# Kernel optimization log

Hardware: AMD Instinct MI355X
Metric: run time of the kernel (lower is better)

Reference implementation:

```python
import jax, jax.numpy as jnp
import numpy as np

B, S, D = 2, 2048, 2048
H, HK, HD = 16, 4, 128          # query heads, kv heads, head dim (H*HD == D)
HID = 4 * D                      # SwiGLU hidden (mult=4)
WIN, SINK = 1024, 4              # sliding window, attention sink tokens
EPS = 1e-6
ROPE_BASE = 10000.0


def rmsnorm(x, g):
    return x * jax.lax.rsqrt(jnp.mean(x * x, axis=-1, keepdims=True) + EPS) * g


def rope_tables(seq_len, head_dim):
    inv = 1.0 / (ROPE_BASE ** (jnp.arange(0, head_dim, 2, dtype=jnp.float32) / head_dim))
    ang = jnp.arange(seq_len, dtype=jnp.float32)[:, None] * inv[None, :]  # [S, HD/2]
    return jnp.cos(ang), jnp.sin(ang)


def apply_rope(x, cos, sin):
    # x: [B, S, h, HD]; rotate-half convention
    x1, x2 = jnp.split(x, 2, axis=-1)
    c = cos[None, :, None, :]
    s = sin[None, :, None, :]
    return jnp.concatenate([x1 * c - x2 * s, x2 * c + x1 * s], axis=-1)


def setup_inputs() -> dict:
    key = jax.random.key(0)
    ks = jax.random.split(key, 10)
    p = 0.02
    return {
        "x": jax.random.normal(ks[0], (B, S, D), dtype=jnp.float32),
        "g1": jnp.ones((D,), dtype=jnp.float32),
        "g2": jnp.ones((D,), dtype=jnp.float32),
        "wq": jax.random.normal(ks[1], (D, H * HD), dtype=jnp.float32) * p,
        "wk": jax.random.normal(ks[2], (D, HK * HD), dtype=jnp.float32) * p,
        "wv": jax.random.normal(ks[3], (D, HK * HD), dtype=jnp.float32) * p,
        "wo": jax.random.normal(ks[4], (H * HD, D), dtype=jnp.float32) * p,
        "w_gate": jax.random.normal(ks[5], (D, HID), dtype=jnp.float32) * p,
        "w_up": jax.random.normal(ks[6], (D, HID), dtype=jnp.float32) * p,
        "w_down": jax.random.normal(ks[7], (HID, D), dtype=jnp.float32) * p,
    }


def reference(x, g1, g2, wq, wk, wv, wo, w_gate, w_up, w_down):
    # ---- pre-norm attention ----
    h = rmsnorm(x, g1)
    q = (h @ wq).reshape(B, S, H, HD)
    k = (h @ wk).reshape(B, S, HK, HD)
    v = (h @ wv).reshape(B, S, HK, HD)

    cos, sin = rope_tables(S, HD)
    q = apply_rope(q, cos, sin)
    k = apply_rope(k, cos, sin)

    # GQA: expand kv heads to query heads
    rep = H // HK
    k = jnp.repeat(k, rep, axis=2)  # [B, S, H, HD]
    v = jnp.repeat(v, rep, axis=2)

    scores = jnp.einsum("bqhd,bkhd->bhqk", q, k) / jnp.sqrt(jnp.float32(HD))

    # causal + sliding-window + attention-sink mask
    i = jnp.arange(S)[:, None]
    j = jnp.arange(S)[None, :]
    allowed = (j <= i) & (((i - j) < WIN) | (j < SINK))  # [S, S]
    scores = jnp.where(allowed[None, None], scores, jnp.float32(-1e9))

    attn = jax.nn.softmax(scores, axis=-1)
    a = jnp.einsum("bhqk,bkhd->bqhd", attn, v).reshape(B, S, H * HD) @ wo

    x = x + a

    # ---- pre-norm SwiGLU FFN ----
    h2 = rmsnorm(x, g2)
    ffn = (jax.nn.silu(h2 @ w_gate) * (h2 @ w_up)) @ w_down
    return x + ffn
```

## Files before the change

### kernel.cpp

```cpp
#include <hip/hip_runtime.h>
#include <hip/hip_bf16.h>
#include <stdint.h>

#define TOK 4096
#define SEQ 2048
#define DM 2048
#define NH 16
#define NKV 4
#define HDIM 128
#define HID 8192
#define WIN 1024
#define SINKN 4

typedef float f32x4 __attribute__((ext_vector_type(4)));
typedef __bf16 bf16x8 __attribute__((ext_vector_type(8)));
typedef unsigned short u16;
typedef unsigned int u32;

#define VM(n) asm volatile("s_waitcnt vmcnt(" #n ")" ::: "memory")
#define LG(n) asm volatile("s_waitcnt lgkmcnt(" #n ")" ::: "memory")
#define SCHED0 __builtin_amdgcn_sched_barrier(0)

__device__ __forceinline__ u16 f2bf(float f) {
  union { float f; u32 u; } v; v.f = f;
  return (u16)((v.u + 0x7fffu + ((v.u >> 16) & 1u)) >> 16);
}
__device__ __forceinline__ float bf2f(u16 h) {
  union { u32 u; float f; } v; v.u = ((u32)h) << 16;
  return v.f;
}
__device__ __forceinline__ f32x4 mfma16(bf16x8 a, bf16x8 b, f32x4 c) {
  return __builtin_amdgcn_mfma_f32_16x16x32_bf16(a, b, c, 0, 0, 0);
}
__device__ __forceinline__ void gld16(const u16* g, u16* l) {
  __builtin_amdgcn_global_load_lds(
      (const __attribute__((address_space(1))) u32*)g,
      (__attribute__((address_space(3))) u32*)l, 16, 0, 0);
}
__device__ __forceinline__ void bar() {
  asm volatile("s_barrier" ::: "memory");
}
__device__ __forceinline__ void swz_rc(int c, int& row, int& k8) {
  row = 2 * (c >> 3) + (((c >> 2) & 1) ^ ((c >> 4) & 1));
  k8 = (c & 3) ^ (row & 3);
}
__device__ __forceinline__ void raster8(int wg, int nwg, int nbx, int& bx, int& by) {
  int cpx = nwg >> 3;
  int s = (wg & 7) * cpx + (wg >> 3);
  by = 8 * (s / (8 * nbx)) + (s & 7);
  bx = (s >> 3) % nbx;
}

__global__ __launch_bounds__(256)
void wtrans(const float* __restrict__ in, u16* __restrict__ out, int K, int N)
{
  __shared__ float t[32][33];
  int tx = threadIdx.x & 31, ty = threadIdx.x >> 5;
  int bx = blockIdx.x, by = blockIdx.y;
  #pragma unroll
  for (int i = 0; i < 4; i++) {
    int r = ty + i * 8;
    t[r][tx] = in[(size_t)(by * 32 + r) * N + bx * 32 + tx];
  }
  __syncthreads();
  #pragma unroll
  for (int i = 0; i < 4; i++) {
    int r = ty + i * 8;
    out[(size_t)(bx * 32 + r) * K + by * 32 + tx] = f2bf(t[tx][r]);
  }
}

__global__ __launch_bounds__(256)
void vtrans(const u16* __restrict__ in, int ld, u16* __restrict__ out)
{
  __shared__ u16 t[32][33];
  int tx = threadIdx.x & 31, ty = threadIdx.x >> 5;
  int bx = blockIdx.x;
  int by = blockIdx.y;
  #pragma unroll
  for (int i = 0; i < 4; i++) {
    int r = ty + i * 8;
    t[r][tx] = in[(size_t)(by * 32 + r) * ld + bx * 32 + tx];
  }
  __syncthreads();
  int b = (by * 32) >> 11;
  int s0 = (by * 32) & (SEQ - 1);
  #pragma unroll
  for (int i = 0; i < 4; i++) {
    int c = bx * 32 + ty + i * 8;
    out[(size_t)(b * (NKV * HDIM) + c) * SEQ + s0 + tx] = t[tx][ty + i * 8];
  }
}

__global__ __launch_bounds__(256)
void rope_table_k(float* __restrict__ ct, float* __restrict__ st)
{
  int idx = blockIdx.x * 256 + threadIdx.x;
  int pos = idx >> 6, d = idx & 63;
  float inv = powf(10000.0f, -(float)d / 64.0f);
  float a = (float)pos * inv;
  ct[idx] = cosf(a);
  st[idx] = sinf(a);
}

__global__ void rope_apply_k(u16* __restrict__ q, int ld,
                             const float* __restrict__ ct,
                             const float* __restrict__ st, float scale)
{
  int t = blockIdx.x;
  int hh = threadIdx.x >> 6;
  int d = threadIdx.x & 63;
  int pos = t & (SEQ - 1);
  size_t base = (size_t)t * ld + hh * HDIM + d;
  float x1 = bf2f(q[base]), x2 = bf2f(q[base + 64]);
  float c = ct[pos * 64 + d], s = st[pos * 64 + d];
  q[base]      = f2bf((x1 * c - x2 * s) * scale);
  q[base + 64] = f2bf((x2 * c + x1 * s) * scale);
}

__global__ __launch_bounds__(256)
void rmsnorm_k(const float* __restrict__ x, const float* __restrict__ g,
               u16* __restrict__ o)
{
  int row = blockIdx.x;
  int tid = threadIdx.x;
  const float* xr = x + (size_t)row * DM;
  float4 v0 = *(const float4*)(xr + tid * 8);
  float4 v1 = *(const float4*)(xr + tid * 8 + 4);
  float ss = v0.x*v0.x + v0.y*v0.y + v0.z*v0.z + v0.w*v0.w
           + v1.x*v1.x + v1.y*v1.y + v1.z*v1.z + v1.w*v1.w;
  #pragma unroll
  for (int d = 1; d < 64; d <<= 1) ss += __shfl_xor(ss, d);
  __shared__ float red[4];
  if ((tid & 63) == 0) red[tid >> 6] = ss;
  __syncthreads();
  float inv = rsqrtf((red[0] + red[1] + red[2] + red[3]) * (1.0f / DM) + 1e-6f);
  float4 g0 = *(const float4*)(g + tid * 8);
  float4 g1 = *(const float4*)(g + tid * 8 + 4);
  ushort4 o0, o1;
  o0.x = f2bf(v0.x * inv * g0.x); o0.y = f2bf(v0.y * inv * g0.y);
  o0.z = f2bf(v0.z * inv * g0.z); o0.w = f2bf(v0.w * inv * g0.w);
  o1.x = f2bf(v1.x * inv * g1.x); o1.y = f2bf(v1.y * inv * g1.y);
  o1.z = f2bf(v1.z * inv * g1.z); o1.w = f2bf(v1.w * inv * g1.w);
  *(ushort4*)(o + (size_t)row * DM + tid * 8) = o0;
  *(ushort4*)(o + (size_t)row * DM + tid * 8 + 4) = o1;
}

template<int EPI>
__global__ __launch_bounds__(512, 1)
void gemmp(const u16* __restrict__ A, const u16* __restrict__ Bt,
           u16* __restrict__ Cb, float* __restrict__ Cf,
           const float* __restrict__ X, int M, int N, int K, int nbx)
{
  constexpr int ASZ = 128 * 64;
  constexpr int SLOT = ASZ + 256 * 64;
  __shared__ u16 lds[3 * SLOT];

  int bx, by;
  raster8(blockIdx.x, gridDim.x, nbx, bx, by);
  int m0 = by * 128;
  int n0 = bx * 256;

  int tid = threadIdx.x;
  int l = tid & 63, w = tid >> 6;
  int l16 = l & 15, lg = l >> 4;
  int wr = w >> 2, wc = w & 3;

  int aoff[4][2], boff[4][2];
  #pragma unroll
  for (int m = 0; m < 4; m++)
    #pragma unroll
    for (int kk = 0; kk < 2; kk++) {
      int row = wr * 64 + m * 16 + l16;
      aoff[m][kk] = ((row * 128 + kk * 64 + lg * 16) ^ ((row & 7) << 4)) >> 1;
    }
  #pragma unroll
  for (int n = 0; n < 4; n++)
    #pragma unroll
    for (int kk = 0; kk < 2; kk++) {
      int br = wc * 64 + n * 16 + l16;
      boff[n][kk] = ASZ + (((br * 128 + kk * 64 + lg * 16) ^ ((br & 7) << 4)) >> 1);
    }

  int urow = tid >> 3;
  int cc = (tid & 7) ^ (urow & 7);
  const u16* pA[2];
  const u16* pB[4];
  pA[0] = A + (size_t)(m0 + urow) * K + cc * 8;
  pA[1] = A + (size_t)(m0 + 64 + urow) * K + cc * 8;
  #pragma unroll
  for (int u = 0; u < 4; u++)
    pB[u] = Bt + (size_t)(n0 + u * 64 + urow) * K + cc * 8;

  const int NT = K >> 6;

  auto stA = [&](int tt, int u) {
    gld16(pA[u] + (size_t)tt * 64, lds + (tt % 3) * SLOT + u * 4096 + tid * 8);
  };
  auto stB = [&](int tt, int u) {
    gld16(pB[u] + (size_t)tt * 64, lds + (tt % 3) * SLOT + ASZ + u * 4096 + tid * 8);
  };

  #pragma unroll
  for (int u = 0; u < 4; u++) stB(0, u);
  stA(0, 0); stA(0, 1);
  #pragma unroll
  for (int u = 0; u < 4; u++) stB(1, u);
  stA(1, 0); stA(1, 1);
  VM(6);
  bar();

  f32x4 acc[4][4];
  f32x4 zero = {0.f, 0.f, 0.f, 0.f};
  #pragma unroll
  for (int m = 0; m < 4; m++)
    #pragma unroll
    for (int n = 0; n < 4; n++) acc[m][n] = zero;

  for (int t = 0; t < NT; ++t) {
    u16* cur = lds + (t % 3) * SLOT;
    const bool st = (t + 2 < NT);

    if (st) { stB(t + 2, 0); stB(t + 2, 1); stB(t + 2, 2); }
    bf16x8 a[4][2], b[2][2], c2[2][2];
    #pragma unroll
    for (int m = 0; m < 4; m++) {
      a[m][0] = *(const bf16x8*)(cur + aoff[m][0]);
      a[m][1] = *(const bf16x8*)(cur + aoff[m][1]);
    }
    #pragma unroll
    for (int n = 0; n < 2; n++) {
      b[n][0] = *(const bf16x8*)(cur + boff[n][0]);
      b[n][1] = *(const bf16x8*)(cur + boff[n][1]);
    }
    SCHED0;
    #pragma unroll
    for (int n = 0; n < 2; n++) {
      c2[n][0] = *(const bf16x8*)(cur + boff[n + 2][0]);
      c2[n][1] = *(const bf16x8*)(cur + boff[n + 2][1]);
    }
    bar();
    LG(4);
    SCHED0;
    __builtin_amdgcn_s_setprio(1);
    #pragma unroll
    for (int m = 0; m < 4; m++)
      #pragma unroll
      for (int n = 0; n < 2; n++) {
        acc[m][n] = mfma16(a[m][0], b[n][0], acc[m][n]);
        acc[m][n] = mfma16(a[m][1], b[n][1], acc[m][n]);
      }
    __builtin_amdgcn_s_setprio(0);
    SCHED0;
    bar();

    if (st) { stB(t + 2, 3); stA(t + 2, 0); stA(t + 2, 1); }
    if (st) { VM(6); }
    else if (t + 1 < NT) { VM(0); }
    bar();
    LG(0);
    SCHED0;
    __builtin_amdgcn_s_setprio(1);
    #pragma unroll
    for (int m = 0; m < 4; m++)
      #pragma unroll
      for (int n = 0; n < 2; n++) {
        acc[m][n + 2] = mfma16(a[m][0], c2[n][0], acc[m][n + 2]);
        acc[m][n + 2] = mfma16(a[m][1], c2[n][1], acc[m][n + 2]);
      }
    __builtin_amdgcn_s_setprio(0);
    SCHED0;
    bar();
  }

  #pragma unroll
  for (int m = 0; m < 4; m++) {
    int row = m0 + wr * 64 + m * 16 + lg * 4;
    #pragma unroll
    for (int n = 0; n < 4; n++) {
      int col = n0 + wc * 64 + n * 16 + l16;
      #pragma unroll
      for (int r = 0; r < 4; r++) {
        size_t idx = (size_t)(row + r) * N + col;
        float v = acc[m][n][r];
        if (EPI == 0) {
          Cb[idx] = f2bf(v);
        } else if (EPI == 1) {
          Cf[idx] = X[idx] + v;
        } else {
          Cf[idx] += v;
        }
      }
    }
  }
}

template<int EPI, int GU, int SPLITK>
__global__ __launch_bounds__(512, 1)
void gemm256(const u16* __restrict__ A, const u16* __restrict__ B1,
             const u16* __restrict__ B2, u16* __restrict__ Cb,
             float* __restrict__ Cf, int Kst, int NT, int N, int nbx)
{
  constexpr int SLOT = 32768;
  __shared__ u16 lds[2 * SLOT];

  int wg = blockIdx.x;
  int nwg = gridDim.x;
  int kh = 0;
  if (SPLITK) { int half = nwg >> 1; kh = (wg >= half); wg -= kh * half; nwg = half; }
  int bx, by;
  raster8(wg, nwg, nbx, bx, by);
  int m0 = by * 256;
  int n0 = bx * (GU ? 128 : 256);
  size_t k0 = (size_t)kh * NT * 64;

  int tid = threadIdx.x;
  int l = tid & 63, w = tid >> 6;
  int l16 = l & 15, lg = l >> 4;
  int wr = w >> 2, wc = w & 3;

  int sw = (l16 & 7) << 4;
  int aoffk[2], boffk[2];
  #pragma unroll
  for (int kk = 0; kk < 2; kk++) {
    aoffk[kk] = ((wr * 128 + l16) * 128 + ((kk * 64 + lg * 16) ^ sw)) >> 1;
    int bbase = GU ? (wc * 32 + l16) : (wc * 64 + l16);
    boffk[kk] = 16384 + (((bbase * 128) + ((kk * 64 + lg * 16) ^ sw)) >> 1);
  }

  int rh = tid >> 3;
  int cc = (tid & 7) ^ (rh & 7);
  const u16* pA0[2]; const u16* pA1[2]; const u16* pB[4];
  #pragma unroll
  for (int ll = 0; ll < 2; ll++) {
    pA0[ll] = A + (size_t)(m0 + ll * 64 + rh) * Kst + k0 + cc * 8;
    pA1[ll] = A + (size_t)(m0 + 128 + ll * 64 + rh) * Kst + k0 + cc * 8;
  }
  #pragma unroll
  for (int u = 0; u < 4; u++) {
    if (GU) pB[u] = (u < 2 ? B1 + (size_t)(n0 + u * 64 + rh) * Kst
                           : B2 + (size_t)(n0 + (u - 2) * 64 + rh) * Kst) + k0 + cc * 8;
    else    pB[u] = B1 + (size_t)(n0 + u * 64 + rh) * Kst + k0 + cc * 8;
  }

  auto stA0 = [&](int tt) {
    u16* d = lds + (tt & 1) * SLOT;
    gld16(pA0[0] + (size_t)tt * 64, d + tid * 8);
    gld16(pA0[1] + (size_t)tt * 64, d + 4096 + tid * 8);
  };
  auto stA1 = [&](int tt) {
    u16* d = lds + (tt & 1) * SLOT + 8192;
    gld16(pA1[0] + (size_t)tt * 64, d + tid * 8);
    gld16(pA1[1] + (size_t)tt * 64, d + 4096 + tid * 8);
  };
  auto stB4 = [&](int tt) {
    u16* d = lds + (tt & 1) * SLOT + 16384;
    #pragma unroll
    for (int u = 0; u < 4; u++)
      gld16(pB[u] + (size_t)tt * 64, d + u * 4096 + tid * 8);
  };

  stA0(0); stA1(0); stB4(0);
  stA0(1); stB4(1);
  VM(6);
  bar();

  f32x4 acc[8][4];
  f32x4 zero = {0.f, 0.f, 0.f, 0.f};
  #pragma unroll
  for (int m = 0; m < 8; m++)
    #pragma unroll
    for (int n = 0; n < 4; n++) acc[m][n] = zero;

  bf16x8 aA[4], aB[4], aC[4], aD[4], bb0[4], bb1[4];
  {
    u16* s0 = lds;
    #pragma unroll
    for (int m = 0; m < 4; m++) aA[m] = *(const bf16x8*)(s0 + aoffk[0] + m * 1024);
    #pragma unroll
    for (int n = 0; n < 4; n++)
      bb0[n] = *(const bf16x8*)(s0 + boffk[0] + (GU ? ((n & 1) * 1024 + (n >> 1) * 8192)
                                                    : (n * 1024)));
  }

  for (int t = 0; t < NT; ++t) {
    u16* cur = lds + (t & 1) * SLOT;
    u16* nxt = lds + ((t + 1) & 1) * SLOT;

    #pragma unroll
    for (int m = 0; m < 4; m++) aB[m] = *(const bf16x8*)(cur + aoffk[0] + 4096 + m * 1024);
    if (t + 1 < NT) stA1(t + 1);
    bar();
    LG(4);
    SCHED0;
    __builtin_amdgcn_s_setprio(1);
    #pragma unroll
    for (int m = 0; m < 4; m++)
      #pragma unroll
      for (int n = 0; n < 4; n++)
        acc[m][n] = mfma16(aA[m], bb0[n], acc[m][n]);
    __builtin_amdgcn_s_setprio(0);
    SCHED0;
    bar();

    #pragma unroll
    for (int m = 0; m < 4; m++) aC[m] = *(const bf16x8*)(cur + aoffk[1] + m * 1024);
    #pragma unroll
    for (int n = 0; n < 4; n++)
      bb1[n] = *(const bf16x8*)(cur + boffk[1] + (GU ? ((n & 1) * 1024 + (n >> 1) * 8192)
                                                     : (n * 1024)));
    bar();
    LG(8);
    SCHED0;
    __builtin_amdgcn_s_setprio(1);
    #pragma unroll
    for (int m = 0; m < 4; m++)
      #pragma unroll
      for (int n = 0; n < 4; n++)
        acc[4 + m][n] = mfma16(aB[m], bb0[n], acc[4 + m][n]);
    __builtin_amdgcn_s_setprio(0);
    SCHED0;
    bar();

    #pragma unroll
    for (int m = 0; m < 4; m++) aD[m] = *(const bf16x8*)(cur + aoffk[1] + 4096 + m * 1024);
    bar();
    LG(0);
    SCHED0;
    __builtin_amdgcn_s_setprio(1);
    #pragma unroll
    for (int m = 0; m < 4; m++)
      #pragma unroll
      for (int n = 0; n < 4; n++)
        acc[m][n] = mfma16(aC[m], bb1[n], acc[m][n]);
    __builtin_amdgcn_s_setprio(0);
    SCHED0;
    bar();

    if (t + 2 < NT) {
      stA0(t + 2); stB4(t + 2);
      VM(6);
    } else if (t + 1 < NT) {
      VM(0);
    }
    bar();
    if (t + 1 < NT) {
      #pragma unroll
      for (int m = 0; m < 4; m++) aA[m] = *(const bf16x8*)(nxt + aoffk[0] + m * 1024);
      #pragma unroll
      for (int n = 0; n < 4; n++)
        bb0[n] = *(const bf16x8*)(nxt + boffk[0] + (GU ? ((n & 1) * 1024 + (n >> 1) * 8192)
                                                       : (n * 1024)));
    }
    LG(8);
    SCHED0;
    __builtin_amdgcn_s_setprio(1);
    #pragma unroll
    for (int m = 0; m < 4; m++)
      #pragma unroll
      for (int n = 0; n < 4; n++)
        acc[4 + m][n] = mfma16(aD[m], bb1[n], acc[4 + m][n]);
    __builtin_amdgcn_s_setprio(0);
    SCHED0;
    bar();
  }

  if (GU) {
    #pragma unroll
    for (int m = 0; m < 8; m++) {
      int row = m0 + wr * 128 + m * 16 + lg * 4;
      #pragma unroll
      for (int n = 0; n < 2; n++) {
        int col = n0 + wc * 32 + n * 16 + l16;
        #pragma unroll
        for (int r = 0; r < 4; r++) {
          float gt = acc[m][n][r];
          float up = acc[m][n + 2][r];
          float sg = gt / (1.0f + __expf(-gt));
          Cb[(size_t)(row + r) * N + col] = f2bf(sg * up);
        }
      }
    }
  } else {
    #pragma unroll
    for (int m = 0; m < 8; m++) {
      int row = m0 + wr * 128 + m * 16 + lg * 4;
      #pragma unroll
      for (int n = 0; n < 4; n++) {
        int col = n0 + wc * 64 + n * 16 + l16;
        #pragma unroll
        for (int r = 0; r < 4; r++) {
          size_t idx = (size_t)(row + r) * N + col;
          if (EPI == 0) Cb[idx] = f2bf(acc[m][n][r]);
          else          atomicAdd(Cf + idx, acc[m][n][r]);
        }
      }
    }
  }
}

__global__ __launch_bounds__(256)
void attn_k(const u16* __restrict__ qb, int ldq,
            const u16* __restrict__ kb, int ldk,
            const u16* __restrict__ vbt, u16* __restrict__ ao)
{
  int q0 = blockIdx.x * 128;
  int h = blockIdx.y;
  int b = blockIdx.z;
  int hk = h >> 2;
  int tid = threadIdx.x;
  int w = tid >> 6, l = tid & 63;
  int l16 = l & 15, lg = l >> 4;

  __shared__ u16 Ks[32 * 128];
  __shared__ u16 Vt[128 * 32];
  __shared__ u16 Ps[4][32 * 40];
  u16* Pw = Ps[w];

  bf16x8 qf[2][4];
  #pragma unroll
  for (int m = 0; m < 2; m++)
    #pragma unroll
    for (int kd = 0; kd < 4; kd++) {
      int row = q0 + w * 32 + m * 16 + l16;
      qf[m][kd] = *(const bf16x8*)(qb + (size_t)(b * SEQ + row) * ldq
                                   + h * HDIM + kd * 32 + lg * 8);
    }

  f32x4 oacc[2][8];
  float mrun[2][4], lrun[2][4];
  f32x4 zero = {0.f, 0.f, 0.f, 0.f};
  #pragma unroll
  for (int m = 0; m < 2; m++) {
    #pragma unroll
    for (int nd = 0; nd < 8; nd++) oacc[m][nd] = zero;
    #pragma unroll
    for (int r = 0; r < 4; r++) { mrun[m][r] = -1e9f; lrun[m][r] = 0.f; }
  }

  int kr0 = tid >> 4,        kc0 = (tid & 15) ^ (kr0 & 7);
  int kr1 = (tid + 256) >> 4, kc1 = (tid & 15) ^ (kr1 & 7);
  int vd0, vk0, vd1, vk1;
  swz_rc(tid, vd0, vk0);
  swz_rc(tid + 256, vd1, vk1);
  const u16* kbase = kb + (size_t)(b * SEQ) * ldk + hk * HDIM;
  const u16* vbase = vbt + (size_t)(b * NKV + hk) * HDIM * SEQ;

  int koff[2][4];
  #pragma unroll
  for (int n = 0; n < 2; n++)
    #pragma unroll
    for (int kd = 0; kd < 4; kd++) {
      int key = n * 16 + l16;
      koff[n][kd] = ((key * 128) + kd * 32 + lg * 8) ^ ((key & 7) * 8);
    }
  int voff[8];
  #pragma unroll
  for (int nd = 0; nd < 8; nd++) {
    int d = nd * 16 + l16;
    voff[nd] = (d * 32 + lg * 8) ^ ((d & 7) * 8);
  }

  int lo = (q0 >= WIN) ? ((q0 - (WIN - 1)) >> 5) : 0;
  int hi = (q0 + 127) >> 5;

  for (int it = (lo > 0 ? lo - 1 : 0); it <= hi; ++it) {
    int kt = (it < lo) ? 0 : it;
    gld16(kbase + (size_t)(kt * 32 + kr0) * ldk + kc0 * 8, Ks + tid * 8);
    gld16(kbase + (size_t)(kt * 32 + kr1) * ldk + kc1 * 8, Ks + (tid + 256) * 8);
    gld16(vbase + (size_t)vd0 * SEQ + kt * 32 + vk0 * 8, Vt + tid * 8);
    gld16(vbase + (size_t)vd1 * SEQ + kt * 32 + vk1 * 8, Vt + (tid + 256) * 8);
    __syncthreads();

    f32x4 sacc[2][2];
    sacc[0][0] = zero; sacc[0][1] = zero; sacc[1][0] = zero; sacc[1][1] = zero;
    #pragma unroll
    for (int kd = 0; kd < 4; kd++) {
      bf16x8 kf0 = *(const bf16x8*)(Ks + koff[0][kd]);
      bf16x8 kf1 = *(const bf16x8*)(Ks + koff[1][kd]);
      #pragma unroll
      for (int m = 0; m < 2; m++) {
        sacc[m][0] = mfma16(qf[m][kd], kf0, sacc[m][0]);
        sacc[m][1] = mfma16(qf[m][kd], kf1, sacc[m][1]);
      }
    }

    #pragma unroll
    for (int m = 0; m < 2; m++) {
      float sc[4];
      #pragma unroll
      for (int r = 0; r < 4; r++) {
        int i = q0 + w * 32 + m * 16 + lg * 4 + r;
        int j0 = kt * 32 + l16;
        int j1 = j0 + 16;
        float s0 = sacc[m][0][r];
        float s1 = sacc[m][1][r];
        bool ok0 = (j0 <= i) && ((i - j0 < WIN) || (j0 < SINKN));
        bool ok1 = (j1 <= i) && ((i - j1 < WIN) || (j1 < SINKN));
        s0 = ok0 ? s0 : -1e9f;
        s1 = ok1 ? s1 : -1e9f;
        float mx = fmaxf(s0, s1);
        mx = fmaxf(mx, __shfl_xor(mx, 1));
        mx = fmaxf(mx, __shfl_xor(mx, 2));
        mx = fmaxf(mx, __shfl_xor(mx, 4));
        mx = fmaxf(mx, __shfl_xor(mx, 8));
        float mold = mrun[m][r];
        float mnew = fmaxf(mold, mx);
        float scl = __expf(mold - mnew);
        mrun[m][r] = mnew;
        float p0 = __expf(s0 - mnew);
        float p1 = __expf(s1 - mnew);
        int prow = m * 16 + lg * 4 + r;
        Pw[prow * 40 + l16] = f2bf(p0);
        Pw[prow * 40 + 16 + l16] = f2bf(p1);
        float ps = p0 + p1;
        ps += __shfl_xor(ps, 1);
        ps += __shfl_xor(ps, 2);
        ps += __shfl_xor(ps, 4);
        ps += __shfl_xor(ps, 8);
        lrun[m][r] = lrun[m][r] * scl + ps;
        sc[r] = scl;
      }
      #pragma unroll
      for (int nd = 0; nd < 8; nd++) {
        oacc[m][nd][0] *= sc[0];
        oacc[m][nd][1] *= sc[1];
        oacc[m][nd][2] *= sc[2];
        oacc[m][nd][3] *= sc[3];
      }
    }

    bf16x8 pa0 = *(const bf16x8*)(Pw + l16 * 40 + lg * 8);
    bf16x8 pa1 = *(const bf16x8*)(Pw + (16 + l16) * 40 + lg * 8);
    #pragma unroll
    for (int nd = 0; nd < 8; nd++) {
      bf16x8 vf = *(const bf16x8*)(Vt + voff[nd]);
      oacc[0][nd] = mfma16(pa0, vf, oacc[0][nd]);
      oacc[1][nd] = mfma16(pa1, vf, oacc[1][nd]);
    }
    __syncthreads();
  }

  #pragma unroll
  for (int m = 0; m < 2; m++)
    #pragma unroll
    for (int r = 0; r < 4; r++) {
      float invl = 1.0f / lrun[m][r];
      int row = q0 + w * 32 + m * 16 + lg * 4 + r;
      #pragma unroll
      for (int nd = 0; nd < 8; nd++) {
        int col = nd * 16 + l16;
        ao[(size_t)(b * SEQ + row) * (NH * HDIM) + h * HDIM + col] =
            f2bf(oacc[m][nd][r] * invl);
      }
    }
}

extern "C" void kernel_launch(void* const* d_in, const int* in_sizes, int n_in,
                              void* d_out, int out_size, void* d_ws, size_t ws_size,
                              hipStream_t stream)
{
  (void)in_sizes; (void)n_in; (void)out_size;
  const float* x  = (const float*)d_in[0];
  const float* g1 = (const float*)d_in[1];
  const float* g2 = (const float*)d_in[2];
  const float* wq = (const float*)d_in[3];
  const float* wk = (const float*)d_in[4];
  const float* wv = (const float*)d_in[5];
  const float* wo = (const float*)d_in[6];
  const float* wg = (const float*)d_in[7];
  const float* wu = (const float*)d_in[8];
  const float* wd = (const float*)d_in[9];
  float* out = (float*)d_out;

  char* ws = (char*)d_ws;
  size_t off = 0;
  auto alloc = [&](size_t bytes) {
    char* p = ws + off;
    off += (bytes + 255) & ~(size_t)255;
    return p;
  };
  const int NQKV = 3072;
  u16* wqkv_t = (u16*)alloc((size_t)NQKV * DM * 2);
  u16* wo_t   = (u16*)alloc((size_t)DM * DM * 2);
  u16* wg_t   = (u16*)alloc((size_t)HID * DM * 2);
  u16* wu_t   = (u16*)alloc((size_t)HID * DM * 2);
  u16* wd_t   = (u16*)alloc((size_t)DM * HID * 2);
  u16* hb     = (u16*)alloc((size_t)TOK * DM * 2);
  char* span0 = ws + off;
  u16* qkvb   = (u16*)alloc((size_t)TOK * NQKV * 2);
  u16* vbt    = (u16*)alloc((size_t)TOK * NKV * HDIM * 2);
  u16* aob    = (u16*)alloc((size_t)TOK * NH * HDIM * 2);
  size_t span_used = (size_t)(ws + off - span0);
  size_t gu_need = (size_t)TOK * HID * 2;
  if (gu_need > span_used) alloc(gu_need - span_used);
  u16* gu = (u16*)span0;
  float* ct  = (float*)alloc((size_t)SEQ * 64 * 4);
  float* st  = (float*)alloc((size_t)SEQ * 64 * 4);
  if (off > ws_size) return;

  dim3 blk(256);
  dim3 blk512(512);

  wtrans<<<dim3(DM / 32, DM / 32), blk, 0, stream>>>(wq, wqkv_t, DM, DM);
  wtrans<<<dim3((NKV * HDIM) / 32, DM / 32), blk, 0, stream>>>(wk, wqkv_t + (size_t)DM * DM, DM, NKV * HDIM);
  wtrans<<<dim3((NKV * HDIM) / 32, DM / 32), blk, 0, stream>>>(wv, wqkv_t + (size_t)(DM + NKV * HDIM) * DM, DM, NKV * HDIM);
  wtrans<<<dim3(DM / 32, DM / 32), blk, 0, stream>>>(wo, wo_t, DM, DM);
  wtrans<<<dim3(HID / 32, DM / 32), blk, 0, stream>>>(wg, wg_t, DM, HID);
  wtrans<<<dim3(HID / 32, DM / 32), blk, 0, stream>>>(wu, wu_t, DM, HID);
  wtrans<<<dim3(DM / 32, HID / 32), blk, 0, stream>>>(wd, wd_t, HID, DM);

  rope_table_k<<<SEQ * 64 / 256, blk, 0, stream>>>(ct, st);
  rmsnorm_k<<<TOK, blk, 0, stream>>>(x, g1, hb);

  gemm256<0, 0, 0><<<dim3((NQKV / 256) * (TOK / 256)), blk512, 0, stream>>>(
      hb, wqkv_t, nullptr, qkvb, nullptr, DM, DM / 64, NQKV, NQKV / 256);

  rope_apply_k<<<TOK, dim3(NH * 64), 0, stream>>>(qkvb, NQKV, ct, st, 0.08838834764831845f);
  rope_apply_k<<<TOK, dim3(NKV * 64), 0, stream>>>(qkvb + DM, NQKV, ct, st, 1.0f);
  vtrans<<<dim3((NKV * HDIM) / 32, TOK / 32), blk, 0, stream>>>(qkvb + DM + NKV * HDIM, NQKV, vbt);

  attn_k<<<dim3(SEQ / 128, NH, 2), blk, 0, stream>>>(qkvb, NQKV, qkvb + DM, NQKV, vbt, aob);

  gemmp<1><<<dim3((DM / 256) * (TOK / 128)), blk512, 0, stream>>>(
      aob, wo_t, nullptr, out, x, TOK, DM, DM, DM / 256);
  rmsnorm_k<<<TOK, blk, 0, stream>>>(out, g2, hb);

  gemm256<0, 1, 0><<<dim3((HID / 128) * (TOK / 256)), blk512, 0, stream>>>(
      hb, wg_t, wu_t, gu, nullptr, DM, DM / 64, HID, HID / 128);

  gemm256<4, 0, 1><<<dim3(2 * (DM / 256) * (TOK / 256)), blk512, 0, stream>>>(
      gu, wd_t, nullptr, nullptr, out, HID, HID / 128, DM, DM / 256);
}
```

Baseline: 781.8 us.

## Restructure GEMM mainloop into quadrant ping-pong with finer-grained LDS staging

```diff
diff --git a/kernel.cpp b/kernel.cpp
--- a/kernel.cpp
+++ b/kernel.cpp
@@ -319,23 +319,29 @@
   int l16 = l & 15, lg = l >> 4;
   int wr = w >> 2, wc = w & 3;
 
-  int sw = (l16 & 7) << 4;
-  int aoffk[2], boffk[2];
-  #pragma unroll
-  for (int kk = 0; kk < 2; kk++) {
-    aoffk[kk] = ((wr * 128 + l16) * 128 + ((kk * 64 + lg * 16) ^ sw)) >> 1;
-    int bbase = GU ? (wc * 32 + l16) : (wc * 64 + l16);
-    boffk[kk] = 16384 + (((bbase * 128) + ((kk * 64 + lg * 16) ^ sw)) >> 1);
-  }
+  int aoff[4][2], boff[2][2];
+  #pragma unroll
+  for (int mm = 0; mm < 4; mm++)
+    #pragma unroll
+    for (int kk = 0; kk < 2; kk++) {
+      int ar = wr * 64 + mm * 16 + l16;
+      aoff[mm][kk] = ((ar * 128 + ((kk * 64 + lg * 16) ^ ((ar & 7) << 4))) >> 1);
+    }
+  #pragma unroll
+  for (int nn = 0; nn < 2; nn++)
+    #pragma unroll
+    for (int kk = 0; kk < 2; kk++) {
+      int br = wc * 32 + nn * 16 + l16;
+      boff[nn][kk] = 16384 + ((br * 128 + ((kk * 64 + lg * 16) ^ ((br & 7) << 4))) >> 1);
+    }
 
   int rh = tid >> 3;
   int cc = (tid & 7) ^ (rh & 7);
-  const u16* pA0[2]; const u16* pA1[2]; const u16* pB[4];
-  #pragma unroll
-  for (int ll = 0; ll < 2; ll++) {
-    pA0[ll] = A + (size_t)(m0 + ll * 64 + rh) * Kst + k0 + cc * 8;
-    pA1[ll] = A + (size_t)(m0 + 128 + ll * 64 + rh) * Kst + k0 + cc * 8;
-  }
+  const u16* pA[4];
+  #pragma unroll
+  for (int u = 0; u < 4; u++)
+    pA[u] = A + (size_t)(m0 + u * 64 + rh) * Kst + k0 + cc * 8;
+  const u16* pB[4];
   #pragma unroll
   for (int u = 0; u < 4; u++) {
     if (GU) pB[u] = (u < 2 ? B1 + (size_t)(n0 + u * 64 + rh) * Kst
@@ -343,25 +349,19 @@
     else    pB[u] = B1 + (size_t)(n0 + u * 64 + rh) * Kst + k0 + cc * 8;
   }
 
-  auto stA0 = [&](int tt) {
-    u16* d = lds + (tt & 1) * SLOT;
-    gld16(pA0[0] + (size_t)tt * 64, d + tid * 8);
-    gld16(pA0[1] + (size_t)tt * 64, d + 4096 + tid * 8);
+  auto stA = [&](int tt, int h) {
+    u16* d = lds + (tt & 1) * SLOT + h * 8192;
+    gld16(pA[h * 2 + 0] + (size_t)tt * 64, d + tid * 8);
+    gld16(pA[h * 2 + 1] + (size_t)tt * 64, d + 4096 + tid * 8);
   };
-  auto stA1 = [&](int tt) {
-    u16* d = lds + (tt & 1) * SLOT + 8192;
-    gld16(pA1[0] + (size_t)tt * 64, d + tid * 8);
-    gld16(pA1[1] + (size_t)tt * 64, d + 4096 + tid * 8);
+  auto stB = [&](int tt, int h) {
+    u16* d = lds + (tt & 1) * SLOT + 16384 + h * 8192;
+    gld16(pB[h * 2 + 0] + (size_t)tt * 64, d + tid * 8);
+    gld16(pB[h * 2 + 1] + (size_t)tt * 64, d + 4096 + tid * 8);
   };
-  auto stB4 = [&](int tt) {
-    u16* d = lds + (tt & 1) * SLOT + 16384;
-    #pragma unroll
-    for (int u = 0; u < 4; u++)
-      gld16(pB[u] + (size_t)tt * 64, d + u * 4096 + tid * 8);
-  };
-
-  stA0(0); stA1(0); stB4(0);
-  stA0(1); stB4(1);
+
+  stA(0, 0); stB(0, 0); stA(0, 1); stB(0, 1);
+  stA(1, 0); stB(1, 0); stA(1, 1);
   VM(6);
   bar();
 
@@ -372,94 +372,91 @@
     #pragma unroll
     for (int n = 0; n < 4; n++) acc[m][n] = zero;
 
-  bf16x8 aA[4], aB[4], aC[4], aD[4], bb0[4], bb1[4];
-  {
-    u16* s0 = lds;
-    #pragma unroll
-    for (int m = 0; m < 4; m++) aA[m] = *(const bf16x8*)(s0 + aoffk[0] + m * 1024);
-    #pragma unroll
-    for (int n = 0; n < 4; n++)
-      bb0[n] = *(const bf16x8*)(s0 + boffk[0] + (GU ? ((n & 1) * 1024 + (n >> 1) * 8192)
-                                                    : (n * 1024)));
-  }
-
   for (int t = 0; t < NT; ++t) {
     u16* cur = lds + (t & 1) * SLOT;
-    u16* nxt = lds + ((t + 1) & 1) * SLOT;
-
-    #pragma unroll
-    for (int m = 0; m < 4; m++) aB[m] = *(const bf16x8*)(cur + aoffk[0] + 4096 + m * 1024);
-    if (t + 1 < NT) stA1(t + 1);
-    bar();
-    LG(4);
+    bf16x8 a0[4][2], a1[4][2], b0[2][2], b1[2][2];
+
+    #pragma unroll
+    for (int mm = 0; mm < 4; mm++)
+      #pragma unroll
+      for (int kk = 0; kk < 2; kk++)
+        a0[mm][kk] = *(const bf16x8*)(cur + aoff[mm][kk]);
+    #pragma unroll
+    for (int nn = 0; nn < 2; nn++)
+      #pragma unroll
+      for (int kk = 0; kk < 2; kk++)
+        b0[nn][kk] = *(const bf16x8*)(cur + boff[nn][kk]);
+    if (t + 1 < NT) stB(t + 1, 1);
+    LG(8);
+    bar();
+    LG(0);
     SCHED0;
     __builtin_amdgcn_s_setprio(1);
     #pragma unroll
-    for (int m = 0; m < 4; m++)
-      #pragma unroll
-      for (int n = 0; n < 4; n++)
-        acc[m][n] = mfma16(aA[m], bb0[n], acc[m][n]);
+    for (int mm = 0; mm < 4; mm++)
+      #pragma unroll
+      for (int nn = 0; nn < 2; nn++)
+        #pragma unroll
+        for (int kk = 0; kk < 2; kk++)
+          acc[mm][nn] = mfma16(a0[mm][kk], b0[nn][kk], acc[mm][nn]);
     __builtin_amdgcn_s_setprio(0);
     SCHED0;
     bar();
 
     #pragma unroll
-    for (int m = 0; m < 4; m++) aC[m] = *(const bf16x8*)(cur + aoffk[1] + m * 1024);
-    #pragma unroll
-    for (int n = 0; n < 4; n++)
-      bb1[n] = *(const bf16x8*)(cur + boffk[1] + (GU ? ((n & 1) * 1024 + (n >> 1) * 8192)
-                                                     : (n * 1024)));
-    bar();
-    LG(8);
+    for (int nn = 0; nn < 2; nn++)
+      #pragma unroll
+      for (int kk = 0; kk < 2; kk++)
+        b1[nn][kk] = *(const bf16x8*)(cur + boff[nn][kk] + 8192);
+    if (t + 2 < NT) stA(t + 2, 0);
+    bar();
+    LG(0);
     SCHED0;
     __builtin_amdgcn_s_setprio(1);
     #pragma unroll
-    for (int m = 0; m < 4; m++)
-      #pragma unroll
-      for (int n = 0; n < 4; n++)
-        acc[4 + m][n] = mfma16(aB[m], bb0[n], acc[4 + m][n]);
+    for (int mm = 0; mm < 4; mm++)
+      #pragma unroll
+      for (int nn = 0; nn < 2; nn++)
+        #pragma unroll
+        for (int kk = 0; kk < 2; kk++)
+          acc[mm][2 + nn] = mfma16(a0[mm][kk], b1[nn][kk], acc[mm][2 + nn]);
     __builtin_amdgcn_s_setprio(0);
     SCHED0;
     bar();
 
     #pragma unroll
-    for (int m = 0; m < 4; m++) aD[m] = *(const bf16x8*)(cur + aoffk[1] + 4096 + m * 1024);
+    for (int mm = 0; mm < 4; mm++)
+      #pragma unroll
+      for (int kk = 0; kk < 2; kk++)
+        a1[mm][kk] = *(const bf16x8*)(cur + aoff[mm][kk] + 8192);
+    if (t + 2 < NT) stB(t + 2, 0);
     bar();
     LG(0);
     SCHED0;
     __builtin_amdgcn_s_setprio(1);
     #pragma unroll
-    for (int m = 0; m < 4; m++)
-      #pragma unroll
-      for (int n = 0; n < 4; n++)
-        acc[m][n] = mfma16(aC[m], bb1[n], acc[m][n]);
+    for (int mm = 0; mm < 4; mm++)
+      #pragma unroll
+      for (int nn = 0; nn < 2; nn++)
+        #pragma unroll
+        for (int kk = 0; kk < 2; kk++)
+          acc[4 + mm][nn] = mfma16(a1[mm][kk], b0[nn][kk], acc[4 + mm][nn]);
     __builtin_amdgcn_s_setprio(0);
     SCHED0;
     bar();
 
-    if (t + 2 < NT) {
-      stA0(t + 2); stB4(t + 2);
-      VM(6);
-    } else if (t + 1 < NT) {
-      VM(0);
-    }
-    bar();
-    if (t + 1 < NT) {
-      #pragma unroll
-      for (int m = 0; m < 4; m++) aA[m] = *(const bf16x8*)(nxt + aoffk[0] + m * 1024);
-      #pragma unroll
-      for (int n = 0; n < 4; n++)
-        bb0[n] = *(const bf16x8*)(nxt + boffk[0] + (GU ? ((n & 1) * 1024 + (n >> 1) * 8192)
-                                                       : (n * 1024)));
-    }
-    LG(8);
+    if (t + 2 < NT) { stA(t + 2, 1); VM(6); }
+    else if (t + 1 < NT) { VM(0); }
+    bar();
     SCHED0;
     __builtin_amdgcn_s_setprio(1);
     #pragma unroll
-    for (int m = 0; m < 4; m++)
-      #pragma unroll
-      for (int n = 0; n < 4; n++)
-        acc[4 + m][n] = mfma16(aD[m], bb1[n], acc[4 + m][n]);
+    for (int mm = 0; mm < 4; mm++)
+      #pragma unroll
+      for (int nn = 0; nn < 2; nn++)
+        #pragma unroll
+        for (int kk = 0; kk < 2; kk++)
+          acc[4 + mm][2 + nn] = mfma16(a1[mm][kk], b1[nn][kk], acc[4 + mm][2 + nn]);
     __builtin_amdgcn_s_setprio(0);
     SCHED0;
     bar();
@@ -468,14 +465,14 @@
   if (GU) {
     #pragma unroll
     for (int m = 0; m < 8; m++) {
-      int row = m0 + wr * 128 + m * 16 + lg * 4;
-      #pragma unroll
-      for (int n = 0; n < 2; n++) {
-        int col = n0 + wc * 32 + n * 16 + l16;
+      int row = m0 + (m >> 2) * 128 + wr * 64 + (m & 3) * 16 + lg * 4;
+      #pragma unroll
+      for (int nn = 0; nn < 2; nn++) {
+        int col = n0 + wc * 32 + nn * 16 + l16;
         #pragma unroll
         for (int r = 0; r < 4; r++) {
-          float gt = acc[m][n][r];
-          float up = acc[m][n + 2][r];
+          float gt = acc[m][nn][r];
+          float up = acc[m][2 + nn][r];
           float sg = gt / (1.0f + __expf(-gt));
           Cb[(size_t)(row + r) * N + col] = f2bf(sg * up);
         }
@@ -484,10 +481,10 @@
   } else {
     #pragma unroll
     for (int m = 0; m < 8; m++) {
-      int row = m0 + wr * 128 + m * 16 + lg * 4;
+      int row = m0 + (m >> 2) * 128 + wr * 64 + (m & 3) * 16 + lg * 4;
       #pragma unroll
       for (int n = 0; n < 4; n++) {
-        int col = n0 + wc * 64 + n * 16 + l16;
+        int col = n0 + (n >> 1) * 128 + wc * 32 + (n & 1) * 16 + l16;
         #pragma unroll
         for (int r = 0; r < 4; r++) {
           size_t idx = (size_t)(row + r) * N + col;
```

Result: no change. 770.9 us (-1.4%).
